# Optimization experiments

Measured on AMD Instinct MI355X. Metric: run time of the kernel, lower is better.

## Reference

```python
import jax, jax.numpy as jnp
import numpy as np

E, K, MULT = 8, 2, 4          # num_experts, top_k, ffn mult
CF = 1.25                     # capacity_factor


def setup_inputs() -> dict:
    key = jax.random.key(0)
    ks = jax.random.split(key, 8)
    B, T, C = 4, 2048, 1024
    H = C * MULT
    s = 0.02
    return {
        "x": jax.random.normal(ks[0], (B, T, C), jnp.float32),
        "rw": jax.random.normal(ks[1], (E, C), jnp.float32) * s,   # router weight [E,C]
        "rb": jnp.zeros((E,), jnp.float32),                        # router bias
        "w1": jax.random.normal(ks[2], (E, C, H), jnp.float32) * s,
        "b1": jnp.zeros((E, H), jnp.float32),
        "w2": jax.random.normal(ks[3], (E, H, C), jnp.float32) * s,
        "b2": jnp.zeros((E, C), jnp.float32),
    }


def reference(x, rw, rb, w1, b1, w2, b2):
    B, T, C = x.shape
    N = B * T
    cap = int(CF * N / E)                      # static capacity per expert
    xf = x.reshape(N, C)
    logits = xf @ rw.T + rb                    # [N,E]
    probs = jax.nn.softmax(logits, axis=-1)
    topk_probs, topk_idx = jax.lax.top_k(probs, K)      # [N,K]
    topk_probs = topk_probs / topk_probs.sum(-1, keepdims=True)

    # Flatten (token, choice) row-major == torch.where(mask) ordering
    flat_idx = topk_idx.reshape(-1)            # [N*K] expert id per slot
    flat_gate = topk_probs.reshape(-1)         # [N*K]
    onehot = jax.nn.one_hot(flat_idx, E, dtype=jnp.int32)          # [N*K,E]
    pos = (jnp.cumsum(onehot, axis=0) - 1)[jnp.arange(N * K), flat_idx]  # rank within expert
    keep = pos < cap                           # first-come-first-served capacity drop
    tok = jnp.arange(N * K) // K               # owning token of each slot

    # Dispatch into [E, cap] buffers; dropped slots go to a dump slot at the end
    buf = jnp.where(keep, flat_idx * cap + pos, E * cap)
    gate_buf = jnp.zeros(E * cap + 1, x.dtype).at[buf].add(flat_gate)[:E * cap]
    tok_buf = jnp.zeros(E * cap + 1, jnp.int32).at[buf].set(tok)[:E * cap]

    inp = xf[tok_buf].reshape(E, cap, C)       # gathered expert inputs
    h = jax.nn.gelu(jnp.einsum('eic,ech->eih', inp, w1) + b1[:, None, :], approximate=False)
    out = jnp.einsum('eih,ehc->eic', h, w2) + b2[:, None, :]
    out = out * gate_buf.reshape(E, cap, 1)    # empty slots have gate 0 -> zero contribution

    y = jnp.zeros((N, C), x.dtype).at[tok_buf].add(out.reshape(E * cap, C))

    # Aux load-balancing loss
    imp = probs.sum(0)
    imp = imp / imp.sum()
    load = jnp.minimum(onehot.sum(0).astype(x.dtype), cap)   # kept token counts
    load = load / load.sum()
    aux_loss = (imp * load).sum() * (E ** 2)
    return y.reshape(B, T, C), aux_loss
```

## Files before the change

### kernel.cpp

```cpp
#include <hip/hip_runtime.h>
#include <hip/hip_bf16.h>
#include <math.h>

#define NE    8
#define KTOP  2
#define CDIM  1024
#define HDIM  4096
#define NTOK  8192
#define CAPE  1280
#define NSLOT (NTOK * KTOP)

typedef __bf16 bf16x8 __attribute__((ext_vector_type(8)));
typedef __bf16 bf16x4 __attribute__((ext_vector_type(4)));
typedef __bf16 bf16x2 __attribute__((ext_vector_type(2)));
typedef float  f32x4  __attribute__((ext_vector_type(4)));

#define GAS __attribute__((address_space(1)))
#define LAS __attribute__((address_space(3)))

__global__ __launch_bounds__(256) void k_transpose_bf16(
    const float* __restrict__ src, __bf16* __restrict__ dst, int R, int Cc)
{
    __shared__ __bf16 T[64][72];
    const int e  = blockIdx.z;
    const int cb = blockIdx.x * 64;
    const int rb = blockIdx.y * 64;
    const int t  = threadIdx.x;
    const int bx = t & 15, by = t >> 4;

    const float* s = src + (size_t)e * R * Cc
                   + (size_t)(rb + by * 4) * Cc + cb + bx * 4;
    float4 m[4];
#pragma unroll
    for (int i = 0; i < 4; ++i)
        m[i] = *(const float4*)(s + (size_t)i * Cc);
#pragma unroll
    for (int j = 0; j < 4; ++j) {
        bf16x4 v;
        v[0] = (__bf16)((&m[0].x)[j]);
        v[1] = (__bf16)((&m[1].x)[j]);
        v[2] = (__bf16)((&m[2].x)[j]);
        v[3] = (__bf16)((&m[3].x)[j]);
        *(bf16x4*)&T[bx * 4 + j][by * 4] = v;
    }
    __syncthreads();
    const int oc = t >> 2, rc = (t & 3) * 16;
    __bf16* d = dst + (size_t)e * R * Cc + (size_t)(cb + oc) * R + rb + rc;
    *(bf16x8*)d       = *(const bf16x8*)&T[oc][rc];
    *(bf16x8*)(d + 8) = *(const bf16x8*)&T[oc][rc + 8];
}

__global__ __launch_bounds__(256) void k_router(
    const float* __restrict__ x, const float* __restrict__ rw,
    const float* __restrict__ rb, float* __restrict__ probs,
    float* __restrict__ gates, int* __restrict__ tidx)
{
    __shared__ float rws[NE * CDIM];
    const int tid = threadIdx.x;
    for (int i = tid; i < NE * CDIM / 4; i += 256)
        ((float4*)rws)[i] = ((const float4*)rw)[i];
    __syncthreads();

    const int wave = tid >> 6, lane = tid & 63;
    const int n = blockIdx.x * 4 + wave;
    const float* xr = x + (size_t)n * CDIM;

    float acc[NE];
#pragma unroll
    for (int e = 0; e < NE; ++e) acc[e] = 0.f;
    for (int j = 0; j < CDIM / 64; ++j) {
        const float xv = xr[j * 64 + lane];
#pragma unroll
        for (int e = 0; e < NE; ++e) acc[e] += xv * rws[e * CDIM + j * 64 + lane];
    }
#pragma unroll
    for (int off = 32; off > 0; off >>= 1) {
#pragma unroll
        for (int e = 0; e < NE; ++e) acc[e] += __shfl_down(acc[e], off);
    }
    if (lane == 0) {
        float mx = -1e30f;
#pragma unroll
        for (int e = 0; e < NE; ++e) { acc[e] += rb[e]; mx = fmaxf(mx, acc[e]); }
        float p[NE], s = 0.f;
#pragma unroll
        for (int e = 0; e < NE; ++e) { p[e] = expf(acc[e] - mx); s += p[e]; }
        const float inv = 1.f / s;
#pragma unroll
        for (int e = 0; e < NE; ++e) { p[e] *= inv; probs[(size_t)n * NE + e] = p[e]; }
        int   i1 = 0;  float v1 = p[0];
        int   i2 = -1; float v2 = -1.f;
#pragma unroll
        for (int e = 1; e < NE; ++e) {
            if (p[e] > v1)      { v2 = v1; i2 = i1; v1 = p[e]; i1 = e; }
            else if (p[e] > v2) { v2 = p[e]; i2 = e; }
        }
        const float gs = 1.f / (v1 + v2);
        gates[n * 2 + 0] = v1 * gs;  gates[n * 2 + 1] = v2 * gs;
        tidx[n * 2 + 0]  = i1;       tidx[n * 2 + 1]  = i2;
    }
}

__global__ __launch_bounds__(256) void k_scan(
    const int* __restrict__ tidx, const float* __restrict__ probs,
    int* __restrict__ slot, int* __restrict__ tok, float* __restrict__ d_aux)
{
    __shared__ int   lcnt[256][NE];
    __shared__ float ps[256][NE];
    const int t = threadIdx.x;

    for (int i = t; i < NE * CAPE; i += 256) tok[i] = 0;

    int c8[NE];
#pragma unroll
    for (int e = 0; e < NE; ++e) c8[e] = 0;
    const int per  = NSLOT / 256;
    const int base = t * per;
    for (int s = 0; s < per; ++s) c8[tidx[base + s]]++;
#pragma unroll
    for (int e = 0; e < NE; ++e) lcnt[t][e] = c8[e];

    float f8[NE];
#pragma unroll
    for (int e = 0; e < NE; ++e) f8[e] = 0.f;
    for (int n = t; n < NTOK; n += 256) {
        const float4 a = *(const float4*)(probs + (size_t)n * NE);
        const float4 b = *(const float4*)(probs + (size_t)n * NE + 4);
        f8[0] += a.x; f8[1] += a.y; f8[2] += a.z; f8[3] += a.w;
        f8[4] += b.x; f8[5] += b.y; f8[6] += b.z; f8[7] += b.w;
    }
#pragma unroll
    for (int e = 0; e < NE; ++e) ps[t][e] = f8[e];

    __syncthreads();

    int pre[NE], tot[NE];
#pragma unroll
    for (int e = 0; e < NE; ++e) { pre[e] = 0; tot[e] = 0; }
    for (int tt = 0; tt < 256; ++tt) {
#pragma unroll
        for (int e = 0; e < NE; ++e) {
            const int v = lcnt[tt][e];
            tot[e] += v;
            if (tt < t) pre[e] += v;
        }
    }
    for (int s = 0; s < per; ++s) {
        const int sg = base + s;
        const int e  = tidx[sg];
        const int p  = pre[e]++;
        if (p < CAPE) { slot[sg] = e * CAPE + p; tok[e * CAPE + p] = sg >> 1; }
        else          { slot[sg] = -1; }
    }
    if (t == 0) {
        float imp[NE], isum = 0.f, ld[NE], lsum = 0.f;
#pragma unroll
        for (int e = 0; e < NE; ++e) {
            float v = 0.f;
            for (int tt = 0; tt < 256; ++tt) v += ps[tt][e];
            imp[e] = v; isum += v;
        }
#pragma unroll
        for (int e = 0; e < NE; ++e) { ld[e] = fminf((float)tot[e], (float)CAPE); lsum += ld[e]; }
        float aux = 0.f;
#pragma unroll
        for (int e = 0; e < NE; ++e) aux += (imp[e] / isum) * (ld[e] / lsum);
        *d_aux = aux * (float)(NE * NE);
    }
}

__global__ __launch_bounds__(256) void k_gather(
    const float* __restrict__ x, const int* __restrict__ tok,
    __bf16* __restrict__ inp)
{
    const int row = blockIdx.x;
    const int t   = threadIdx.x;
    const int tk  = tok[row];
    const float4 v = ((const float4*)(x + (size_t)tk * CDIM))[t];
    bf16x4 o;
    o[0] = (__bf16)v.x; o[1] = (__bf16)v.y; o[2] = (__bf16)v.z; o[3] = (__bf16)v.w;
    *(bf16x4*)(inp + (size_t)row * CDIM + t * 4) = o;
}

#define MFMA_BF16 __builtin_amdgcn_mfma_f32_16x16x32_bf16
#define DSR_I(dst, addr, IMM) \
    asm volatile("ds_read_b128 %0, %1 offset:" #IMM : "=v"(dst) : "v"(addr))
#define DSR(dst, addr, IMM) DSR_I(dst, addr, IMM)
#define WVM4() asm volatile("s_waitcnt vmcnt(4)" ::: "memory")
#define SB0()  __builtin_amdgcn_sched_barrier(0)

#define PH(RDB, OA0, OA1, MB, VA0, VA1, VB0, VB1, STG, VMW)                   \
    {                                                                         \
        if (RDB) {                                                            \
            DSR(fb[0][0], VB0, 0);    DSR(fb[0][1], VB1, 0);                  \
            DSR(fb[1][0], VB0, 2048); DSR(fb[1][1], VB1, 2048);               \
            DSR(fb[2][0], VB0, 4096); DSR(fb[2][1], VB1, 4096);               \
            DSR(fb[3][0], VB0, 6144); DSR(fb[3][1], VB1, 6144);               \
        }                                                                     \
        DSR(fa[0][0], VA0, OA0); DSR(fa[0][1], VA1, OA0);                     \
        DSR(fa[1][0], VA0, OA1); DSR(fa[1][1], VA1, OA1);                     \
        STG;                                                                  \
        if (RDB) { asm volatile("s_waitcnt lgkmcnt(8)" ::: "memory"); }       \
        __builtin_amdgcn_s_barrier();                                         \
        asm volatile("s_waitcnt lgkmcnt(0)" ::: "memory");                    \
        SB0();                                                                \
        __builtin_amdgcn_s_setprio(1);                                        \
        _Pragma("unroll")                                                     \
        for (int n = 0; n < 4; ++n) {                                         \
            acc[MB][n]   = MFMA_BF16(fb[n][0], fa[0][0], acc[MB][n], 0,0,0);  \
            acc[MB][n]   = MFMA_BF16(fb[n][1], fa[0][1], acc[MB][n], 0,0,0);  \
            acc[MB+1][n] = MFMA_BF16(fb[n][0], fa[1][0], acc[MB+1][n],0,0,0); \
            acc[MB+1][n] = MFMA_BF16(fb[n][1], fa[1][1], acc[MB+1][n],0,0,0); \
        }                                                                     \
        __builtin_amdgcn_s_setprio(0);                                        \
        VMW;                                                                  \
        __builtin_amdgcn_s_barrier();                                        \
        SB0();                                                                \
    }

template <bool GELU>
__global__ __launch_bounds__(512, 2) void k_gemm8(
    const __bf16* __restrict__ Aall, const __bf16* __restrict__ Ball,
    const float* __restrict__ biasAll, __bf16* __restrict__ Call,
    int Ktot, int Ntot, int NBN, int mtPerE)
{
    __shared__ char lds[131072];

    const int NK  = Ktot >> 6;
    const int NI  = NK >> 1;
    const int cpx = gridDim.x >> 3;
    const int id  = blockIdx.x;
    const int sid = (id & 7) * cpx + (id >> 3);
    const int bm  = sid / NBN, bn = sid % NBN;
    const int e   = bm / mtPerE;

    const size_t row0 = (size_t)bm * 256;
    const int    col0 = bn * 256;

    const int tid = threadIdx.x;
    const int w   = tid >> 6, l = tid & 63;
    const int wr  = w >> 2, wc = w & 3;
    const int lr  = l & 15, hi = l >> 4;

    const int srow = tid >> 3;
    const int kf   = ((tid & 7) ^ (srow & 7)) << 3;
    const __bf16* pA = Aall + (row0 + srow) * (size_t)Ktot + kf;
    const __bf16* pB = Ball + ((size_t)e * Ntot + col0 + srow) * (size_t)Ktot + kf;
    const unsigned L0 = (unsigned)(size_t)(LAS char*)lds;

    const unsigned sA00 = L0 +          w * 1024;
    const unsigned sA01 = sA00 + 16384;
    const unsigned sA10 = sA00 + 32768;
    const unsigned sA11 = sA00 + 49152;
    const unsigned sB00 = sA00 + 65536;
    const unsigned sB01 = sB00 + 16384;
    const unsigned sB10 = sB00 + 32768;
    const unsigned sB11 = sB00 + 49152;

    auto SH_A = [&](unsigned dbase, int half, int kt) {
        const __bf16* g = pA + (size_t)(half * 128) * Ktot + (size_t)kt * 64;
#pragma unroll
        for (int gg = 0; gg < 2; ++gg)
            __builtin_amdgcn_global_load_lds(
                (const GAS void*)(g + (size_t)gg * 64 * Ktot),
                (LAS void*)(size_t)(dbase + gg * 8192), 16, 0, 0);
    };
    auto SH_B = [&](unsigned dbase, int half, int kt) {
        const __bf16* g = pB + (size_t)(half * 128) * Ktot + (size_t)kt * 64;
#pragma unroll
        for (int gg = 0; gg < 2; ++gg)
            __builtin_amdgcn_global_load_lds(
                (const GAS void*)(g + (size_t)gg * 64 * Ktot),
                (LAS void*)(size_t)(dbase + gg * 8192), 16, 0, 0);
    };

    const unsigned swz = (l & 7) << 4;
    const unsigned kb0 = ((unsigned)(hi << 4)) ^ swz;
    const unsigned kb1 = ((unsigned)(64 + (hi << 4))) ^ swz;
    const unsigned vA00 = L0 + (unsigned)(wr * 16384 + lr * 128) + kb0;
    const unsigned vA01 = L0 + (unsigned)(wr * 16384 + lr * 128) + kb1;
    const unsigned vA10 = vA00 + 32768, vA11 = vA01 + 32768;
    const unsigned vBb  = L0 + 65536
        + (unsigned)((wc >> 1) * 16384 + ((wc & 1) * 64 + lr) * 128);
    const unsigned vB00 = vBb + kb0, vB01 = vBb + kb1;
    const unsigned vB10 = vB00 + 32768, vB11 = vB01 + 32768;

    SH_B(sB00, 0, 0); SH_B(sB01, 1, 0);
    SH_A(sA00, 0, 0); SH_A(sA01, 1, 0);
    SH_B(sB10, 0, 1); SH_B(sB11, 1, 1);
    WVM4();
    __builtin_amdgcn_s_barrier();
    SB0();

    f32x4 acc[8][4] = {};
    bf16x8 fa[2][2], fb[4][2];

    for (int i = 0; i < NI; ++i) {
        const int t1 = 2 * i + 1;
        const int t2 = (2 * i + 2 < NK) ? 2 * i + 2 : NK - 1;
        const int t3 = (2 * i + 3 < NK) ? 2 * i + 3 : NK - 1;
        PH(1, 0,     2048,  0, vA00, vA01, vB00, vB01, SH_A(sA10, 0, t1), (void)0)
        PH(0, 4096,  6144,  2, vA00, vA01, vB00, vB01, SH_A(sA11, 1, t1), (void)0)
        PH(0, 8192,  10240, 4, vA00, vA01, vB00, vB01, SH_B(sB00, 0, t2), (void)0)
        PH(0, 12288, 14336, 6, vA00, vA01, vB00, vB01, SH_B(sB01, 1, t2), WVM4())
        PH(1, 0,     2048,  0, vA10, vA11, vB10, vB11, SH_A(sA00, 0, t2), (void)0)
        PH(0, 4096,  6144,  2, vA10, vA11, vB10, vB11, SH_A(sA01, 1, t2), (void)0)
        PH(0, 8192,  10240, 4, vA10, vA11, vB10, vB11, SH_B(sB10, 0, t3), (void)0)
        PH(0, 12288, 14336, 6, vA10, vA11, vB10, vB11, SH_B(sB11, 1, t3), WVM4())
    }

    const size_t crow0 = row0 + (size_t)wr * 128;
    const int    ccol0 = col0 + wc * 64;
#pragma unroll
    for (int n = 0; n < 4; ++n) {
        float bbv[4] = {0.f, 0.f, 0.f, 0.f};
        if (GELU) {
            const float4 b4 = *(const float4*)(biasAll + (size_t)e * Ntot
                                               + ccol0 + n * 16 + hi * 4);
            bbv[0] = b4.x; bbv[1] = b4.y; bbv[2] = b4.z; bbv[3] = b4.w;
        }
#pragma unroll
        for (int m = 0; m < 8; ++m) {
            const f32x4 v = acc[m][n];
            bf16x4 o;
#pragma unroll
            for (int i = 0; i < 4; ++i) {
                float t = v[i];
                if (GELU) {
                    t += bbv[i];
                    const float u  = 0.7978845608028654f * (t + 0.044715f * t * t * t);
                    const float ex = __expf(2.f * u);
                    t = t * (1.f - 1.f / (ex + 1.f));
                }
                o[i] = (__bf16)t;
            }
            *(bf16x4*)(Call + (crow0 + m * 16 + lr) * (size_t)Ntot
                       + ccol0 + n * 16 + hi * 4) = o;
        }
    }
}

__global__ __launch_bounds__(256) void k_combine(
    const __bf16* __restrict__ outb, const int* __restrict__ slot,
    const float* __restrict__ gates, const int* __restrict__ tidx,
    const float* __restrict__ b2, float* __restrict__ y)
{
    const int n = blockIdx.x;
    const int t = threadIdx.x;
    const int c = t * 4;
    float r0 = 0.f, r1 = 0.f, r2 = 0.f, r3 = 0.f;
#pragma unroll
    for (int k = 0; k < KTOP; ++k) {
        const int s = slot[n * 2 + k];
        if (s < 0) continue;
        const float g = gates[n * 2 + k];
        const int   e = tidx[n * 2 + k];
        const bf16x4 v = *(const bf16x4*)(outb + (size_t)s * CDIM + c);
        const float4 bb = *(const float4*)(b2 + (size_t)e * CDIM + c);
        r0 += g * ((float)v[0] + bb.x);
        r1 += g * ((float)v[1] + bb.y);
        r2 += g * ((float)v[2] + bb.z);
        r3 += g * ((float)v[3] + bb.w);
    }
    float4 o = make_float4(r0, r1, r2, r3);
    *(float4*)(y + (size_t)n * CDIM + c) = o;
}

extern "C" void kernel_launch(void* const* d_in, const int* in_sizes, int n_in,
                              void* d_out, int out_size, void* d_ws, size_t ws_size,
                              hipStream_t stream)
{
    const float* x  = (const float*)d_in[0];
    const float* rw = (const float*)d_in[1];
    const float* rb = (const float*)d_in[2];
    const float* w1 = (const float*)d_in[3];
    const float* b1 = (const float*)d_in[4];
    const float* w2 = (const float*)d_in[5];
    const float* b2 = (const float*)d_in[6];
    float* y = (float*)d_out;

    char* ws = (char*)d_ws;
    size_t off = 0;
    auto alloc = [&](size_t bytes) -> void* {
        void* p = ws + off;
        off = (off + bytes + 255) & ~(size_t)255;
        return p;
    };
    __bf16* w1t  = (__bf16*)alloc((size_t)NE * CDIM * HDIM * 2);
    __bf16* w2t  = (__bf16*)alloc((size_t)NE * CDIM * HDIM * 2);
    __bf16* inp  = (__bf16*)alloc((size_t)NE * CAPE * CDIM * 2);
    __bf16* hbuf = (__bf16*)alloc((size_t)NE * CAPE * HDIM * 2);
    __bf16* outb = (__bf16*)alloc((size_t)NE * CAPE * CDIM * 2);
    float*  probs = (float*)alloc((size_t)NTOK * NE * 4);
    float*  gates = (float*)alloc((size_t)NTOK * 2 * 4);
    int*    tidx  = (int*)alloc((size_t)NTOK * 2 * 4);
    int*    slot  = (int*)alloc((size_t)NTOK * 2 * 4);
    int*    tok   = (int*)alloc((size_t)NE * CAPE * 4);

    k_transpose_bf16<<<dim3(HDIM / 64, CDIM / 64, NE), 256, 0, stream>>>(
        w1, w1t, CDIM, HDIM);
    k_transpose_bf16<<<dim3(CDIM / 64, HDIM / 64, NE), 256, 0, stream>>>(
        w2, w2t, HDIM, CDIM);

    k_router<<<NTOK / 4, 256, 0, stream>>>(x, rw, rb, probs, gates, tidx);

    k_scan<<<1, 256, 0, stream>>>(tidx, probs, slot, tok, y + (size_t)NTOK * CDIM);

    k_gather<<<NE * CAPE, 256, 0, stream>>>(x, tok, inp);

    k_gemm8<true><<<dim3((NE * CAPE / 256) * (HDIM / 256)), 512, 0, stream>>>(
        inp, w1t, b1, hbuf, CDIM, HDIM, HDIM / 256, CAPE / 256);
    k_gemm8<false><<<dim3((NE * CAPE / 256) * (CDIM / 256)), 512, 0, stream>>>(
        hbuf, w2t, nullptr, outb, HDIM, CDIM, CDIM / 256, CAPE / 256);

    k_combine<<<NTOK, 256, 0, stream>>>(outb, slot, gates, tidx, b2, y);
}
```

Measured before the change: 413.3 us.

## Stage GEMM epilogue through LDS for coalesced stores; parallelize routing scans

The GEMM epilogue now writes the bf16 output tile into LDS using a padded row stride, then stores it to global memory with wide 16-byte rows so the writes coalesce. The old path used scattered 8-byte stores. The LDS allocation grows slightly to hold the padded tile, which may affect the two-blocks-per-CU occupancy. Separately, the routing kernel replaces its serial 256-iteration prefix count and importance sums with a Hillis-Steele scan and a tree reduction, which adds several barriers.

New measurement: 381.8 us. -7.6%, faster.

```diff
diff --git a/kernel.cpp b/kernel.cpp
--- a/kernel.cpp
+++ b/kernel.cpp
@@ -134,17 +134,33 @@
 
     __syncthreads();
 
+    int run[NE];
+#pragma unroll
+    for (int e = 0; e < NE; ++e) run[e] = c8[e];
+    for (int d = 1; d < 256; d <<= 1) {
+        int add[NE];
+#pragma unroll
+        for (int e = 0; e < NE; ++e) add[e] = (t >= d) ? lcnt[t - d][e] : 0;
+        __syncthreads();
+#pragma unroll
+        for (int e = 0; e < NE; ++e) { run[e] += add[e]; lcnt[t][e] = run[e]; }
+        __syncthreads();
+    }
     int pre[NE], tot[NE];
 #pragma unroll
-    for (int e = 0; e < NE; ++e) { pre[e] = 0; tot[e] = 0; }
-    for (int tt = 0; tt < 256; ++tt) {
-#pragma unroll
-        for (int e = 0; e < NE; ++e) {
-            const int v = lcnt[tt][e];
-            tot[e] += v;
-            if (tt < t) pre[e] += v;
+    for (int e = 0; e < NE; ++e) {
+        pre[e] = run[e] - c8[e];
+        tot[e] = lcnt[255][e];
+    }
+
+    for (int d = 128; d >= 1; d >>= 1) {
+        if (t < d) {
+#pragma unroll
+            for (int e = 0; e < NE; ++e) ps[t][e] += ps[t + d][e];
         }
-    }
+        __syncthreads();
+    }
+
     for (int s = 0; s < per; ++s) {
         const int sg = base + s;
         const int e  = tidx[sg];
@@ -153,18 +169,14 @@
         else          { slot[sg] = -1; }
     }
     if (t == 0) {
-        float imp[NE], isum = 0.f, ld[NE], lsum = 0.f;
-#pragma unroll
-        for (int e = 0; e < NE; ++e) {
-            float v = 0.f;
-            for (int tt = 0; tt < 256; ++tt) v += ps[tt][e];
-            imp[e] = v; isum += v;
-        }
+        float isum = 0.f, lsum = 0.f, ld[NE];
+#pragma unroll
+        for (int e = 0; e < NE; ++e) isum += ps[0][e];
 #pragma unroll
         for (int e = 0; e < NE; ++e) { ld[e] = fminf((float)tot[e], (float)CAPE); lsum += ld[e]; }
         float aux = 0.f;
 #pragma unroll
-        for (int e = 0; e < NE; ++e) aux += (imp[e] / isum) * (ld[e] / lsum);
+        for (int e = 0; e < NE; ++e) aux += (ps[0][e] / isum) * (ld[e] / lsum);
         *d_aux = aux * (float)(NE * NE);
     }
 }
@@ -224,7 +236,7 @@
     const float* __restrict__ biasAll, __bf16* __restrict__ Call,
     int Ktot, int Ntot, int NBN, int mtPerE)
 {
-    __shared__ char lds[131072];
+    __shared__ char lds[133120];
 
     const int NK  = Ktot >> 6;
     const int NI  = NK >> 1;
@@ -309,14 +321,18 @@
         PH(0, 12288, 14336, 6, vA10, vA11, vB10, vB11, SH_B(sB11, 1, t3), WVM4())
     }
 
-    const size_t crow0 = row0 + (size_t)wr * 128;
-    const int    ccol0 = col0 + wc * 64;
+    asm volatile("s_waitcnt vmcnt(0)" ::: "memory");
+    __builtin_amdgcn_s_barrier();
+    SB0();
+
+    const int lrow0 = wr * 128;
+    const int lcol0 = wc * 64;
 #pragma unroll
     for (int n = 0; n < 4; ++n) {
         float bbv[4] = {0.f, 0.f, 0.f, 0.f};
         if (GELU) {
             const float4 b4 = *(const float4*)(biasAll + (size_t)e * Ntot
-                                               + ccol0 + n * 16 + hi * 4);
+                                               + col0 + lcol0 + n * 16 + hi * 4);
             bbv[0] = b4.x; bbv[1] = b4.y; bbv[2] = b4.z; bbv[3] = b4.w;
         }
 #pragma unroll
@@ -334,8 +350,20 @@
                 }
                 o[i] = (__bf16)t;
             }
-            *(bf16x4*)(Call + (crow0 + m * 16 + lr) * (size_t)Ntot
-                       + ccol0 + n * 16 + hi * 4) = o;
+            *(bf16x4*)(lds + (lrow0 + m * 16 + lr) * 520
+                           + (lcol0 + n * 16 + hi * 4) * 2) = o;
+        }
+    }
+    __builtin_amdgcn_s_barrier();
+
+    {
+        const int rr0 = tid >> 5;
+        const int cc  = (tid & 31) * 8;
+#pragma unroll
+        for (int it = 0; it < 16; ++it) {
+            const int rr = it * 16 + rr0;
+            const bf16x8 v = *(const bf16x8*)(lds + rr * 520 + cc * 2);
+            *(bf16x8*)(Call + (row0 + rr) * (size_t)Ntot + col0 + cc) = v;
         }
     }
 }
```
